# Optimization experiments

Measured on AMD Instinct MI355X. Metric: run time of the kernel, lower is better.

The kernel has to match this reference:

```python
import jax, jax.numpy as jnp
import numpy as np

B, CIN, COUT, H, W, KK = 1, 32, 64, 181, 360, 4
NNZ_PER, NNZ_PER1 = 9, 4


def _make_psi(rng, K, H, W, nnz_per):
    # Sparse DISCO basis in COO form for longitude 0 (shift-invariant in lon).
    E = K * H * nnz_per
    seg = np.repeat(np.arange(K * H, dtype=np.int32), nnz_per)  # k*H + ho
    ho = seg % H
    dlat = rng.integers(-1, 2, size=E).astype(np.int32)
    hi = np.clip(ho + dlat, 0, H - 1).astype(np.int32)
    wi = (rng.integers(-1, 2, size=E).astype(np.int32)) % W
    vals = (rng.normal(size=E) * 0.2).astype(np.float32)
    return seg, hi, wi, vals


def setup_inputs() -> dict:
    rng = np.random.default_rng(0)
    key = jax.random.key(0)
    ks = jax.random.split(key, 5)
    x = jax.random.normal(ks[0], (B, CIN, H, W), dtype=jnp.float32)
    # spherical quadrature weights: sin(colatitude) * cell area
    theta = np.linspace(0.0, np.pi, H)
    qw = (np.sin(theta) * (np.pi / (H - 1)) * (2.0 * np.pi / W)).astype(np.float32)
    qw = np.maximum(qw, 1e-8).reshape(H, 1)
    seg, hi, wi, vals = _make_psi(rng, KK, H, W, NNZ_PER)
    seg1, hi1, wi1, vals1 = _make_psi(rng, 1, H, W, NNZ_PER1)
    w_depth = jax.random.normal(ks[1], (CIN, KK), dtype=jnp.float32) / np.sqrt(KK)
    w_point = jax.random.normal(ks[2], (COUT, CIN), dtype=jnp.float32) / np.sqrt(CIN)
    bias = jax.random.normal(ks[3], (COUT,), dtype=jnp.float32) * 0.02
    return {
        "x": x,
        "quad_w": jnp.asarray(qw),
        "vals": jnp.asarray(vals),
        "seg": jnp.asarray(seg),
        "hi": jnp.asarray(hi),
        "wi": jnp.asarray(wi),
        "w_depth": w_depth,
        "vals1": jnp.asarray(vals1),
        "seg1": jnp.asarray(seg1),
        "hi1": jnp.asarray(hi1),
        "wi1": jnp.asarray(wi1),
        "w_point": w_point,
        "bias": bias,
        "K": KK,
    }


def _disco_contract(x, vals, seg, hi, wi, K):
    # x: [B,C,H,W]; COO psi at lon 0; out[b,c,k,ho,wo] =
    #   sum_{e: seg[e]==k*H+ho} vals[e] * x[b,c,hi[e],(wi[e]+wo) mod W]
    Bq, C, Hq, Wq = x.shape
    rows = x[:, :, hi, :]                                        # [B,C,E,W]
    col = (wi[:, None] + jnp.arange(Wq, dtype=wi.dtype)[None, :]) % Wq  # [E,W]
    rolled = jnp.take_along_axis(rows, col[None, None, :, :], axis=3)   # [B,C,E,W]
    weighted = rolled * vals[None, None, :, None]
    out = jax.ops.segment_sum(weighted.transpose(2, 0, 1, 3), seg,
                              num_segments=K * Hq)               # [K*H,B,C,W]
    return out.reshape(K, Hq, Bq, C, Wq).transpose(2, 3, 0, 1, 4)  # [B,C,K,H,W]


def reference(x, quad_w, vals, seg, hi, wi, w_depth, vals1, seg1, hi1, wi1,
              w_point, bias, K):
    # depthwise DISCO conv (groups=C_in, no bias)
    xq = x * quad_w                                   # quadrature weighting
    xd = _disco_contract(xq, vals, seg, hi, wi, K)    # [B,C,K,H,W]
    y = jnp.einsum("ck,bckhw->bchw", w_depth, xd)     # per-channel K mix
    # pointwise DISCO conv (kernel_shape=1) = CLinear
    yq = y * quad_w
    z = _disco_contract(yq, vals1, seg1, hi1, wi1, 1)[:, :, 0]  # [B,C,H,W]
    out = jnp.einsum("oc,bchw->bohw", w_point, z) + bias[None, :, None, None]
    return out
```

## Files before the change

kernel.cpp:

```cpp
#include <hip/hip_runtime.h>


#define H_    181
#define W_    360
#define CIN_  32
#define COUT_ 64
#define K_    4
#define NNZ_  9
#define NNZ1_ 4
#define HW_   (H_*W_)
#define NT_   (NNZ1_*K_*NNZ_)
#define PXT_  128

__global__ __launch_bounds__(256) void sepconv_stencil(
    const float* __restrict__ x, const float* __restrict__ quad_w,
    const float* __restrict__ vals, const int* __restrict__ hi,
    const int* __restrict__ wi, const float* __restrict__ w_depth,
    const float* __restrict__ vals1, const int* __restrict__ hi1,
    const int* __restrict__ wi1, float* __restrict__ z)
{
    const int bx = blockIdx.x;
    const int h  = (bx & 7) * 23 + (bx >> 3);
    if (h >= H_) return;
    const int cseg = blockIdx.y;
    const int tid  = threadIdx.x;

    __shared__ float Tval[NT_];
    __shared__ int   Tbin[NT_];
    __shared__ float S[K_][25];
    __shared__ float C[4][25];

    if (tid < NT_) {
        const int a   = tid / 36;
        const int rem = tid - a * 36;
        const int k   = rem / 9;
        const int j   = rem - k * 9;
        const int e1  = h * NNZ1_ + a;
        const int m   = hi1[e1];
        const int w1  = wi1[e1];
        const int d1  = (w1 == 1) ? 1 : ((w1 == 0) ? 0 : -1);
        const int e   = (k * H_ + m) * NNZ_ + j;
        const int r   = hi[e];
        const int w0  = wi[e];
        const int d   = (w0 == 1) ? 1 : ((w0 == 0) ? 0 : -1);
        Tval[tid] = vals1[e1] * quad_w[m] * vals[e] * quad_w[r];
        Tbin[tid] = (r - h + 2) * 5 + (d1 + d + 2);
    }
    __syncthreads();

    if (tid < K_ * 25) {
        const int k   = tid / 25;
        const int bin = tid - k * 25;
        float s = 0.f;
        #pragma unroll
        for (int a = 0; a < NNZ1_; ++a)
            #pragma unroll
            for (int j = 0; j < NNZ_; ++j) {
                const int t2 = a * 36 + k * 9 + j;
                if (Tbin[t2] == bin) s += Tval[t2];
            }
        S[k][bin] = s;
    }
    __syncthreads();

    if (tid < 4 * 25) {
        const int c4  = tid / 25;
        const int bin = tid - c4 * 25;
        const int c   = cseg * 4 + c4;
        float acc = 0.f;
        #pragma unroll
        for (int k = 0; k < K_; ++k) acc += w_depth[c * K_ + k] * S[k][bin];
        C[c4][bin] = acc;
    }
    __syncthreads();

    int rowoff[5];
    #pragma unroll
    for (int rb = 0; rb < 5; ++rb) {
        int r = h - 2 + rb;
        r = (r < 0) ? 0 : ((r > H_ - 1) ? H_ - 1 : r);
        rowoff[rb] = r * W_;
    }

    for (int item = tid; item < 4 * 90; item += 256) {
        const int c4 = item / 90;
        const int g  = item - c4 * 90;
        const int c  = cseg * 4 + c4;
        const int bw = g * 4;
        const int cA = (bw + W_ - 4) % W_;
        const int cB = bw;
        const int cC = (bw + 4) % W_;
        const float* xc = x + c * HW_;
        const float* Cc = &C[c4][0];

        float a0 = 0.f, a1 = 0.f, a2 = 0.f, a3 = 0.f;
        #pragma unroll
        for (int rb = 0; rb < 5; ++rb) {
            const float* xr = xc + rowoff[rb];
            const float4 vA = *(const float4*)(xr + cA);
            const float4 vB = *(const float4*)(xr + cB);
            const float4 vC = *(const float4*)(xr + cC);
            const float k0 = Cc[rb * 5 + 0], k1 = Cc[rb * 5 + 1],
                        k2 = Cc[rb * 5 + 2], k3 = Cc[rb * 5 + 3],
                        k4 = Cc[rb * 5 + 4];
            a0 += k0 * vA.z + k1 * vA.w + k2 * vB.x + k3 * vB.y + k4 * vB.z;
            a1 += k0 * vA.w + k1 * vB.x + k2 * vB.y + k3 * vB.z + k4 * vB.w;
            a2 += k0 * vB.x + k1 * vB.y + k2 * vB.z + k3 * vB.w + k4 * vC.x;
            a3 += k0 * vB.y + k1 * vB.z + k2 * vB.w + k3 * vC.x + k4 * vC.y;
        }
        float4 r4; r4.x = a0; r4.y = a1; r4.z = a2; r4.w = a3;
        *(float4*)(z + c * HW_ + h * W_ + bw) = r4;
    }
}

__global__ __launch_bounds__(256) void sepconv_pointwise(
    const float* __restrict__ z, const float* __restrict__ w_point,
    const float* __restrict__ bias, float* __restrict__ out)
{
    const int p0  = blockIdx.x * PXT_;
    const int tid = threadIdx.x;

    __shared__ float zs[CIN_][PXT_];
    for (int i = tid; i < CIN_ * PXT_; i += 256) {
        const int c = i >> 7;
        const int j = i & (PXT_ - 1);
        const int p = p0 + j;
        zs[c][j] = (p < HW_) ? z[c * HW_ + p] : 0.f;
    }
    __syncthreads();

    const int j  = tid & (PXT_ - 1);
    const int oh = tid >> 7;
    const int p  = p0 + j;

    float zr[CIN_];
    #pragma unroll
    for (int c = 0; c < CIN_; ++c) zr[c] = zs[c][j];

    if (p < HW_) {
        const float* wp = w_point + oh * 32 * CIN_;
        float* op = out + oh * 32 * HW_ + p;
        #pragma unroll 8
        for (int oo = 0; oo < 32; ++oo) {
            float acc = bias[oh * 32 + oo];
            #pragma unroll
            for (int c = 0; c < CIN_; ++c) acc += wp[oo * CIN_ + c] * zr[c];
            op[oo * HW_] = acc;
        }
    }
}

extern "C" void kernel_launch(void* const* d_in, const int* in_sizes, int n_in,
                              void* d_out, int out_size, void* d_ws, size_t ws_size,
                              hipStream_t stream) {
    const float* x       = (const float*)d_in[0];
    const float* quad_w  = (const float*)d_in[1];
    const float* vals    = (const float*)d_in[2];
    const int*   hi      = (const int*)d_in[4];
    const int*   wi      = (const int*)d_in[5];
    const float* w_depth = (const float*)d_in[6];
    const float* vals1   = (const float*)d_in[7];
    const int*   hi1     = (const int*)d_in[9];
    const int*   wi1     = (const int*)d_in[10];
    const float* w_point = (const float*)d_in[11];
    const float* bias    = (const float*)d_in[12];

    float* z = (float*)d_ws;

    sepconv_stencil<<<dim3(184, 8), 256, 0, stream>>>(
        x, quad_w, vals, hi, wi, w_depth, vals1, hi1, wi1, z);
    sepconv_pointwise<<<(HW_ + PXT_ - 1) / PXT_, 256, 0, stream>>>(
        z, w_point, bias, (float*)d_out);
}
```

Measured before the change: 125.7 us.

## Split stencil coefficient build into separate kernel and shrink pointwise pixel tile

```diff
diff --git a/kernel.cpp b/kernel.cpp
--- a/kernel.cpp
+++ b/kernel.cpp
@@ -10,25 +10,22 @@
 #define NNZ1_ 4
 #define HW_   (H_*W_)
 #define NT_   (NNZ1_*K_*NNZ_)
-#define PXT_  128
+#define CSTRIDE_ (H_*25)
+#define PXT_  64
 
-__global__ __launch_bounds__(256) void sepconv_stencil(
-    const float* __restrict__ x, const float* __restrict__ quad_w,
+__global__ __launch_bounds__(256) void sepconv_coefs(
+    const float* __restrict__ quad_w,
     const float* __restrict__ vals, const int* __restrict__ hi,
     const int* __restrict__ wi, const float* __restrict__ w_depth,
     const float* __restrict__ vals1, const int* __restrict__ hi1,
-    const int* __restrict__ wi1, float* __restrict__ z)
+    const int* __restrict__ wi1, float* __restrict__ Call)
 {
-    const int bx = blockIdx.x;
-    const int h  = (bx & 7) * 23 + (bx >> 3);
-    if (h >= H_) return;
-    const int cseg = blockIdx.y;
-    const int tid  = threadIdx.x;
+    const int h   = blockIdx.x;
+    const int tid = threadIdx.x;
 
     __shared__ float Tval[NT_];
     __shared__ int   Tbin[NT_];
     __shared__ float S[K_][25];
-    __shared__ float C[4][25];
 
     if (tid < NT_) {
         const int a   = tid / 36;
@@ -63,14 +60,31 @@
     }
     __syncthreads();
 
-    if (tid < 4 * 25) {
-        const int c4  = tid / 25;
-        const int bin = tid - c4 * 25;
-        const int c   = cseg * 4 + c4;
+    for (int item = tid; item < CIN_ * 25; item += 256) {
+        const int c   = item / 25;
+        const int bin = item - c * 25;
         float acc = 0.f;
         #pragma unroll
         for (int k = 0; k < K_; ++k) acc += w_depth[c * K_ + k] * S[k][bin];
-        C[c4][bin] = acc;
+        Call[c * CSTRIDE_ + h * 25 + bin] = acc;
+    }
+}
+
+__global__ __launch_bounds__(256) void sepconv_stencil(
+    const float* __restrict__ x, const float* __restrict__ Call,
+    float* __restrict__ z)
+{
+    const int bx = blockIdx.x;
+    const int h  = (bx & 7) * 23 + (bx >> 3);
+    if (h >= H_) return;
+    const int cseg = blockIdx.y;
+    const int tid  = threadIdx.x;
+
+    __shared__ float C[4][25];
+    if (tid < 100) {
+        const int c4  = tid / 25;
+        const int bin = tid - c4 * 25;
+        C[c4][bin] = Call[(cseg * 4 + c4) * CSTRIDE_ + h * 25 + bin];
     }
     __syncthreads();
 
@@ -121,8 +135,9 @@
     const int tid = threadIdx.x;
 
     __shared__ float zs[CIN_][PXT_];
+    #pragma unroll
     for (int i = tid; i < CIN_ * PXT_; i += 256) {
-        const int c = i >> 7;
+        const int c = i >> 6;
         const int j = i & (PXT_ - 1);
         const int p = p0 + j;
         zs[c][j] = (p < HW_) ? z[c * HW_ + p] : 0.f;
@@ -130,23 +145,22 @@
     __syncthreads();
 
     const int j  = tid & (PXT_ - 1);
-    const int oh = tid >> 7;
+    const int oh = tid >> 6;
     const int p  = p0 + j;
+    if (p >= HW_) return;
 
     float zr[CIN_];
     #pragma unroll
     for (int c = 0; c < CIN_; ++c) zr[c] = zs[c][j];
 
-    if (p < HW_) {
-        const float* wp = w_point + oh * 32 * CIN_;
-        float* op = out + oh * 32 * HW_ + p;
-        #pragma unroll 8
-        for (int oo = 0; oo < 32; ++oo) {
-            float acc = bias[oh * 32 + oo];
-            #pragma unroll
-            for (int c = 0; c < CIN_; ++c) acc += wp[oo * CIN_ + c] * zr[c];
-            op[oo * HW_] = acc;
-        }
+    const float* wp = w_point + oh * 16 * CIN_;
+    float* op = out + oh * 16 * HW_ + p;
+    #pragma unroll 4
+    for (int oo = 0; oo < 16; ++oo) {
+        float acc = bias[oh * 16 + oo];
+        #pragma unroll
+        for (int c = 0; c < CIN_; ++c) acc += wp[oo * CIN_ + c] * zr[c];
+        op[oo * HW_] = acc;
     }
 }
 
@@ -165,10 +179,12 @@
     const float* w_point = (const float*)d_in[11];
     const float* bias    = (const float*)d_in[12];
 
-    float* z = (float*)d_ws;
+    float* Call = (float*)d_ws;
+    float* z    = (float*)((char*)d_ws + (1 << 20));
 
-    sepconv_stencil<<<dim3(184, 8), 256, 0, stream>>>(
-        x, quad_w, vals, hi, wi, w_depth, vals1, hi1, wi1, z);
+    sepconv_coefs<<<H_, 256, 0, stream>>>(
+        quad_w, vals, hi, wi, w_depth, vals1, hi1, wi1, Call);
+    sepconv_stencil<<<dim3(184, 8), 256, 0, stream>>>(x, Call, z);
     sepconv_pointwise<<<(HW_ + PXT_ - 1) / PXT_, 256, 0, stream>>>(
         z, w_point, bias, (float*)d_out);
 }
```

Measured after the change: 128.1 us. No clear change (+1.9%).
